# Kernel tuning notes

Measured on AMD Instinct MI355X. Metric: run time of the kernel, lower is better.

The kernel has to match this reference:

```python
import jax, jax.numpy as jnp
import numpy as np

B, NEW_S, RES_S, H = 8, 2048, 4096, 1024


def setup_inputs() -> dict:
    key = jax.random.key(0)
    k1, k2, k3 = jax.random.split(key, 3)
    hidden_states = jax.random.normal(k1, (B, NEW_S, H), dtype=jnp.float32)
    residual_hidden_states = jax.random.normal(k2, (B, RES_S, H), dtype=jnp.float32)
    # per-token repeat counts in {1,2}; cumsum <= 2*NEW_S == RES_S so indices are in range
    merged_embeddings_counts = jax.random.randint(k3, (B, NEW_S), 1, 3, dtype=jnp.int64)
    attention_mask = jnp.ones((B, NEW_S), dtype=jnp.int32)
    residual_attention_mask = jnp.ones((B, RES_S), dtype=jnp.int32)
    return {
        "hidden_states": hidden_states,
        "attention_mask": attention_mask,
        "merged_embeddings_counts": merged_embeddings_counts,
        "residual_hidden_states": residual_hidden_states,
        "residual_attention_mask": residual_attention_mask,
    }


def reference(hidden_states, attention_mask, merged_embeddings_counts,
              residual_hidden_states, residual_attention_mask):
    # Vectorized form of the original per-token loop:
    #   restored[b, cumsum(counts)[b,i]-1] += hidden[b,i]
    # with the loop breaking at the first zero count (cumprod mask).
    counts = merged_embeddings_counts  # [B, NEW_S] int
    valid = jnp.cumprod((counts > 0).astype(jnp.int32), axis=1).astype(bool)  # break at first 0
    idx = jnp.cumsum(counts, axis=1) - 1  # [B, NEW_S] scatter target in residual seq
    contrib = jnp.where(valid[..., None], hidden_states, 0.0)  # zero out tokens after break
    res_s = residual_hidden_states.shape[1]
    idx = jnp.where(valid, idx, res_s)  # OOB index -> dropped by mode='drop'
    b_idx = jnp.arange(hidden_states.shape[0])[:, None]  # [B,1]
    restored = residual_hidden_states.at[b_idx, idx].add(contrib, mode="drop")
    return restored
```

## Files before the change

kernel.cpp:

```cpp
#include <hip/hip_runtime.h>
#include <hip/hip_bf16.h>

#define BB     8
#define NEW_S  2048
#define RES_S  4096
#define HDIM   1024
#define H4     (HDIM / 4)

#define TPB    256
#define NBLK   2048
#define NROWS  (BB * RES_S)
#define ITERS  (NROWS / NBLK)

typedef float f4 __attribute__((ext_vector_type(4)));

__global__ __launch_bounds__(1024) void build_inv_kernel(
    const int* __restrict__ counts, int* __restrict__ inv) {
    const int b = blockIdx.x;
    const int t = threadIdx.x;
    int* invb = inv + b * RES_S;

#pragma unroll
    for (int k = 0; k < RES_S / 1024; ++k) invb[t + k * 1024] = -1;
    __syncthreads();

    const int* cb = counts + b * NEW_S;
    const int c0 = cb[2 * t];
    const int c1 = cb[2 * t + 1];

    const unsigned long long e0 =
        (unsigned long long)(unsigned)(c0 > 0 ? c0 : 0) |
        ((unsigned long long)(c0 <= 0) << 32);
    const unsigned long long e1 =
        (unsigned long long)(unsigned)(c1 > 0 ? c1 : 0) |
        ((unsigned long long)(c1 <= 0) << 32);
    const unsigned long long p = e0 + e1;

    const int lane = t & 63;
    const int wave = t >> 6;
    unsigned long long x = p;
#pragma unroll
    for (int d = 1; d < 64; d <<= 1) {
        unsigned long long y = __shfl_up(x, d, 64);
        if (lane >= d) x += y;
    }

    __shared__ unsigned long long wsum[16];
    if (lane == 63) wsum[wave] = x;
    __syncthreads();
    if (t == 0) {
        unsigned long long acc = 0;
#pragma unroll
        for (int w = 0; w < 16; ++w) {
            unsigned long long v = wsum[w];
            wsum[w] = acc;
            acc += v;
        }
    }
    __syncthreads();

    const unsigned long long excl  = wsum[wave] + (x - p);
    const unsigned long long incl0 = excl + e0;
    const unsigned long long incl1 = incl0 + e1;

    if ((incl0 >> 32) == 0ULL) {
        const int idx = (int)(incl0 & 0xffffffffULL) - 1;
        if (idx >= 0 && idx < RES_S) invb[idx] = 2 * t;
    }
    if ((incl1 >> 32) == 0ULL) {
        const int idx = (int)(incl1 & 0xffffffffULL) - 1;
        if (idx >= 0 && idx < RES_S) invb[idx] = 2 * t + 1;
    }
}

__global__ __launch_bounds__(256) void fanout_add_kernel(
    const f4* __restrict__ hidden,
    const f4* __restrict__ residual,
    const int* __restrict__ inv,
    f4* __restrict__ out) {
    const int t   = threadIdx.x;
    const int blk = blockIdx.x;

    int src[ITERS];
#pragma unroll
    for (int k = 0; k < ITERS; ++k)
        src[k] = __builtin_amdgcn_readfirstlane(inv[blk + k * NBLK]);

#pragma unroll 8
    for (int k = 0; k < ITERS; ++k) {
        const int row   = blk + k * NBLK;
        const size_t e  = (size_t)row * H4 + t;
        f4 r = residual[e];
        if (src[k] >= 0) {
            const int b = row >> 12;
            r += hidden[((size_t)(b << 11) + src[k]) * H4 + t];
        }
        __builtin_nontemporal_store(r, &out[e]);
    }
}

extern "C" void kernel_launch(void* const* d_in, const int* in_sizes, int n_in,
                              void* d_out, int out_size, void* d_ws, size_t ws_size,
                              hipStream_t stream) {
    const float* hidden   = (const float*)d_in[0];
    const int*   counts   = (const int*)d_in[2];
    const float* residual = (const float*)d_in[3];
    float* out = (float*)d_out;

    int* inv = (int*)d_ws;

    build_inv_kernel<<<BB, 1024, 0, stream>>>(counts, inv);
    fanout_add_kernel<<<NBLK, TPB, 0, stream>>>(
        (const f4*)hidden, (const f4*)residual, inv, (f4*)out);
}
```

Before: 62.04 us.

## Fuse inverse-index scan into fanout kernel with blockwise rows and software-pipelined loads

Removes the separate build_inv kernel and its workspace round-trip. Each block now redoes the per-batch prefix scan over counts (8 per thread via int4 loads) and keeps only its 16 contiguous rows' source indices in LDS. The fanout loop is double-buffered with sched_barriers so loads of one group overlap stores of the previous one. Hidden rows are loaded unconditionally, with index 0 as a fallback, and masked afterwards. This trades one launch and a dependency for redundant scan work in every block and extra hidden traffic on rows with no source.

```diff
diff --git a/kernel.cpp b/kernel.cpp
--- a/kernel.cpp
+++ b/kernel.cpp
@@ -4,99 +4,125 @@
 #define BB     8
 #define NEW_S  2048
 #define RES_S  4096
-#define HDIM   1024
-#define H4     (HDIM / 4)
-
+#define H4     256
 #define TPB    256
-#define NBLK   2048
-#define NROWS  (BB * RES_S)
-#define ITERS  (NROWS / NBLK)
+#define RPB    16
+#define NBLK   (BB * RES_S / RPB)
+#define GRP    2
 
 typedef float f4 __attribute__((ext_vector_type(4)));
 
-__global__ __launch_bounds__(1024) void build_inv_kernel(
-    const int* __restrict__ counts, int* __restrict__ inv) {
-    const int b = blockIdx.x;
-    const int t = threadIdx.x;
-    int* invb = inv + b * RES_S;
+__global__ __launch_bounds__(TPB, 8) void fanout_fused_kernel(
+    const f4* __restrict__ hidden,
+    const f4* __restrict__ residual,
+    const int* __restrict__ counts,
+    f4* __restrict__ out) {
 
+    const int t   = threadIdx.x;
+    const int blk = blockIdx.x;
+    const int bb  = blk >> 8;
+    const int r0  = (blk & 255) * RPB;
+
+    __shared__ int src_lds[RPB];
+    __shared__ unsigned long long wsum[4];
+
+    if (t < RPB) src_lds[t] = -1;
+
+    const int4* cb4 = (const int4*)(counts + bb * NEW_S);
+    const int4 ca = cb4[2 * t];
+    const int4 cb = cb4[2 * t + 1];
+    const int c[8] = {ca.x, ca.y, ca.z, ca.w, cb.x, cb.y, cb.z, cb.w};
+    unsigned long long e[8], p = 0;
 #pragma unroll
-    for (int k = 0; k < RES_S / 1024; ++k) invb[t + k * 1024] = -1;
-    __syncthreads();
-
-    const int* cb = counts + b * NEW_S;
-    const int c0 = cb[2 * t];
-    const int c1 = cb[2 * t + 1];
-
-    const unsigned long long e0 =
-        (unsigned long long)(unsigned)(c0 > 0 ? c0 : 0) |
-        ((unsigned long long)(c0 <= 0) << 32);
-    const unsigned long long e1 =
-        (unsigned long long)(unsigned)(c1 > 0 ? c1 : 0) |
-        ((unsigned long long)(c1 <= 0) << 32);
-    const unsigned long long p = e0 + e1;
-
-    const int lane = t & 63;
-    const int wave = t >> 6;
+    for (int j = 0; j < 8; ++j) {
+        e[j] = (unsigned long long)(unsigned)(c[j] > 0 ? c[j] : 0) |
+               ((unsigned long long)(c[j] <= 0) << 32);
+        p += e[j];
+    }
+    const int lane = t & 63, wave = t >> 6;
     unsigned long long x = p;
 #pragma unroll
     for (int d = 1; d < 64; d <<= 1) {
         unsigned long long y = __shfl_up(x, d, 64);
         if (lane >= d) x += y;
     }
-
-    __shared__ unsigned long long wsum[16];
     if (lane == 63) wsum[wave] = x;
     __syncthreads();
     if (t == 0) {
         unsigned long long acc = 0;
 #pragma unroll
-        for (int w = 0; w < 16; ++w) {
-            unsigned long long v = wsum[w];
-            wsum[w] = acc;
-            acc += v;
+        for (int w = 0; w < 4; ++w) {
+            const unsigned long long v = wsum[w];
+            wsum[w] = acc; acc += v;
+        }
+    }
+    __syncthreads();
+    unsigned long long acc = wsum[wave] + (x - p);
+#pragma unroll
+    for (int j = 0; j < 8; ++j) {
+        acc += e[j];
+        if ((acc >> 32) == 0ULL) {
+            const int l = (int)(acc & 0xffffffffULL) - 1 - r0;
+            if (l >= 0 && l < RPB) src_lds[l] = 8 * t + j;
         }
     }
     __syncthreads();
 
-    const unsigned long long excl  = wsum[wave] + (x - p);
-    const unsigned long long incl0 = excl + e0;
-    const unsigned long long incl1 = incl0 + e1;
+    int srcv[RPB];
+#pragma unroll
+    for (int k = 0; k < RPB; ++k)
+        srcv[k] = __builtin_amdgcn_readfirstlane(src_lds[k]);
 
-    if ((incl0 >> 32) == 0ULL) {
-        const int idx = (int)(incl0 & 0xffffffffULL) - 1;
-        if (idx >= 0 && idx < RES_S) invb[idx] = 2 * t;
+    const size_t rbase = ((size_t)bb * RES_S + r0) * H4 + t;
+    const size_t hbase = ((size_t)bb * NEW_S) * H4 + t;
+
+    f4 rA[GRP], hA[GRP], rB[GRP], hB[GRP];
+
+#define LOADG(g, rr, hh)                                                 \
+    _Pragma("unroll")                                                    \
+    for (int j = 0; j < GRP; ++j) {                                      \
+        const int k = (g) * GRP + j;                                     \
+        rr[j] = residual[rbase + (size_t)k * H4];                        \
+        const int s = srcv[k] >= 0 ? srcv[k] : 0;     \
+        hh[j] = hidden[hbase + (size_t)s * H4];                          \
     }
-    if ((incl1 >> 32) == 0ULL) {
-        const int idx = (int)(incl1 & 0xffffffffULL) - 1;
-        if (idx >= 0 && idx < RES_S) invb[idx] = 2 * t + 1;
+
+#define CONSUME(g, rr, hh)                                               \
+    _Pragma("unroll")                                                    \
+    for (int j = 0; j < GRP; ++j) {                                      \
+        const int k = (g) * GRP + j;                                     \
+        f4 v = rr[j];                                                    \
+        const f4 z = {0.f, 0.f, 0.f, 0.f};                               \
+        v += (srcv[k] >= 0) ? hh[j] : z;                    \
+        __builtin_nontemporal_store(v, &out[rbase + (size_t)k * H4]);    \
     }
-}
 
-__global__ __launch_bounds__(256) void fanout_add_kernel(
-    const f4* __restrict__ hidden,
-    const f4* __restrict__ residual,
-    const int* __restrict__ inv,
-    f4* __restrict__ out) {
-    const int t   = threadIdx.x;
-    const int blk = blockIdx.x;
+    LOADG(0, rA, hA);
+    LOADG(1, rB, hB);
+    __builtin_amdgcn_sched_barrier(0);
+    CONSUME(0, rA, hA);
+    LOADG(2, rA, hA);
+    __builtin_amdgcn_sched_barrier(0);
+    CONSUME(1, rB, hB);
+    LOADG(3, rB, hB);
+    __builtin_amdgcn_sched_barrier(0);
+    CONSUME(2, rA, hA);
+    LOADG(4, rA, hA);
+    __builtin_amdgcn_sched_barrier(0);
+    CONSUME(3, rB, hB);
+    LOADG(5, rB, hB);
+    __builtin_amdgcn_sched_barrier(0);
+    CONSUME(4, rA, hA);
+    LOADG(6, rA, hA);
+    __builtin_amdgcn_sched_barrier(0);
+    CONSUME(5, rB, hB);
+    LOADG(7, rB, hB);
+    __builtin_amdgcn_sched_barrier(0);
+    CONSUME(6, rA, hA);
+    CONSUME(7, rB, hB);
 
-    int src[ITERS];
-#pragma unroll
-    for (int k = 0; k < ITERS; ++k)
-        src[k] = __builtin_amdgcn_readfirstlane(inv[blk + k * NBLK]);
-
-#pragma unroll 8
-    for (int k = 0; k < ITERS; ++k) {
-        const int row   = blk + k * NBLK;
-        const size_t e  = (size_t)row * H4 + t;
-        f4 r = residual[e];
-        if (src[k] >= 0) {
-            const int b = row >> 12;
-            r += hidden[((size_t)(b << 11) + src[k]) * H4 + t];
-        }
-        __builtin_nontemporal_store(r, &out[e]);
-    }
+#undef LOADG
+#undef CONSUME
 }
 
 extern "C" void kernel_launch(void* const* d_in, const int* in_sizes, int n_in,
@@ -107,9 +133,6 @@
     const float* residual = (const float*)d_in[3];
     float* out = (float*)d_out;
 
-    int* inv = (int*)d_ws;
-
-    build_inv_kernel<<<BB, 1024, 0, stream>>>(counts, inv);
-    fanout_add_kernel<<<NBLK, TPB, 0, stream>>>(
-        (const f4*)hidden, (const f4*)residual, inv, (f4*)out);
+    fanout_fused_kernel<<<NBLK, TPB, 0, stream>>>(
+        (const f4*)hidden, (const f4*)residual, counts, (f4*)out);
 }
```

Result: faster. 54.11 us (-12.8%).
